# Kernel optimization log

Measured on AMD Instinct MI355X. Metric: run time of the kernel, lower is better.

Reference implementation:

```python
import jax, jax.numpy as jnp
import numpy as np

B, E, N, D = 1024, 64, 32, 64  # batch, entities, sampled neighbors, dim


def setup_inputs() -> dict:
    key = jax.random.key(0)
    ks = jax.random.split(key, 6)
    return {
        "self_vectors": jax.random.normal(ks[0], (B, E, 1, D), dtype=jnp.float32),
        "neighbor_vectors": jax.random.normal(ks[1], (B, E, N, D), dtype=jnp.float32),
        "neighbor_relations": jax.random.normal(ks[2], (B, E, N, D), dtype=jnp.float32),
        "user_embeddings": jax.random.normal(ks[3], (B, D), dtype=jnp.float32),
        "W": jax.random.normal(ks[4], (D, 2 * D), dtype=jnp.float32) * (1.0 / np.sqrt(2 * D)),
        "b": jax.random.normal(ks[5], (D,), dtype=jnp.float32) * 0.01,
    }


def reference(self_vectors, neighbor_vectors, neighbor_relations, user_embeddings, W, b):
    # per-neighbor relation scores: (u . r) over dim -> [B, E, N]
    scores = jnp.einsum("bd,bend->ben", user_embeddings, neighbor_relations)
    p = jax.nn.softmax(scores, axis=-1)  # over neighbors
    # weighted neighbor sum -> [B, E, D]
    neighbors_agg = jnp.einsum("ben,bend->bed", p, neighbor_vectors)
    # 'concat' aggregator: cat(self, agg) on feature axis -> [B*E, 2D]
    sv = self_vectors.reshape(B, E, D)
    output = jnp.concatenate([sv, neighbors_agg], axis=-1).reshape(-1, 2 * D)
    output = output @ W.T + b  # Linear(2D -> D)
    return jax.nn.relu(output).reshape(B, -1, D)  # act = ReLU (inner KGCN layers)
```

## Files before the change

kernel.cpp:

```cpp
#include <hip/hip_runtime.h>
#include <math.h>

#define NB  1024
#define NE  64
#define NN  32
#define ND  64

__global__ __launch_bounds__(256) void kgcn_agg_kernel(
    const float* __restrict__ self_v,
    const float* __restrict__ nbr_v,
    const float* __restrict__ nbr_r,
    const float* __restrict__ user,
    const float* __restrict__ W,
    const float* __restrict__ bias,
    float* __restrict__ out)
{
    const int pair = blockIdx.x;
    const int b    = pair >> 6;
    const int t    = threadIdx.x;

    __shared__ float4 s_u4[16];
    __shared__ float4 s_x4[32];
    __shared__ float  s_scores[NN];
    __shared__ float  s_p[NN];
    __shared__ float4 s_part4[256];

    float* s_u    = (float*)s_u4;
    float* s_x    = (float*)s_x4;
    float* s_part = (float*)s_part4;

    if (t < 64) {
        s_u[t] = user[b * ND + t];
    } else if (t < 128) {
        s_x[t - 64] = self_v[(size_t)pair * ND + (t - 64)];
    }
    __syncthreads();

    const float4* rel4 = (const float4*)(nbr_r + (size_t)pair * (NN * ND));
    const float4* nv4  = (const float4*)(nbr_v + (size_t)pair * (NN * ND));

    const int col = t & 15;
    const int rg  = t >> 4;
    const int n_a = rg;
    const int n_b = rg + 16;

    float4 u4 = s_u4[col];

    float4 ra = rel4[t];
    float4 rb = rel4[t + 256];
    float4 va = nv4[t];
    float4 vb = nv4[t + 256];

    float pa = ra.x * u4.x + ra.y * u4.y + ra.z * u4.z + ra.w * u4.w;
    float pb = rb.x * u4.x + rb.y * u4.y + rb.z * u4.z + rb.w * u4.w;

    #pragma unroll
    for (int off = 8; off > 0; off >>= 1) {
        pa += __shfl_down(pa, off, 16);
        pb += __shfl_down(pb, off, 16);
    }
    if (col == 0) {
        s_scores[n_a] = pa;
        s_scores[n_b] = pb;
    }
    __syncthreads();

    if (t < 32) {
        float v = s_scores[t];
        float m = v;
        #pragma unroll
        for (int off = 16; off > 0; off >>= 1)
            m = fmaxf(m, __shfl_xor(m, off, 32));
        float e = __expf(v - m);
        float s = e;
        #pragma unroll
        for (int off = 16; off > 0; off >>= 1)
            s += __shfl_xor(s, off, 32);
        s_p[t] = e / s;
    }
    __syncthreads();

    float p_a = s_p[n_a];
    float p_b = s_p[n_b];
    float4 acc;
    acc.x = p_a * va.x + p_b * vb.x;
    acc.y = p_a * va.y + p_b * vb.y;
    acc.z = p_a * va.z + p_b * vb.z;
    acc.w = p_a * va.w + p_b * vb.w;
    s_part4[rg * 16 + col] = acc;
    __syncthreads();

    if (t < 64) {
        float a = 0.f;
        #pragma unroll
        for (int g = 0; g < 16; ++g)
            a += s_part[g * 64 + t];
        s_x[64 + t] = a;
    }
    __syncthreads();

    const int dout = t >> 2;
    const int q    = t & 3;
    const float4* W4 = (const float4*)W;
    float acc2 = 0.f;
    #pragma unroll
    for (int i = 0; i < 8; ++i) {
        float4 w = W4[dout * 32 + q * 8 + i];
        float4 x = s_x4[q * 8 + i];
        acc2 += w.x * x.x + w.y * x.y + w.z * x.z + w.w * x.w;
    }
    acc2 += __shfl_down(acc2, 2, 4);
    acc2 += __shfl_down(acc2, 1, 4);
    if (q == 0) {
        float r = acc2 + bias[dout];
        out[(size_t)pair * ND + dout] = fmaxf(r, 0.f);
    }
}

extern "C" void kernel_launch(void* const* d_in, const int* in_sizes, int n_in,
                              void* d_out, int out_size, void* d_ws, size_t ws_size,
                              hipStream_t stream) {
    const float* self_v = (const float*)d_in[0];
    const float* nbr_v  = (const float*)d_in[1];
    const float* nbr_r  = (const float*)d_in[2];
    const float* user   = (const float*)d_in[3];
    const float* W      = (const float*)d_in[4];
    const float* bias   = (const float*)d_in[5];
    float* out          = (float*)d_out;

    const int n_pairs = NB * NE;
    kgcn_agg_kernel<<<n_pairs, 256, 0, stream>>>(
        self_v, nbr_v, nbr_r, user, W, bias, out);
}
```

Before: 1.097 ms.

## Map one wavefront per entity pair and drop block-level barriers

Each 64-lane wavefront now handles one (batch, entity) pair, with four pairs per 256-thread block. Scores, softmax and the weighted sum are done in registers with cross-lane shuffles instead of shared-memory staging and several __syncthreads. Each lane loads 16 float4 values, which raises memory-level parallelism but also register pressure. The linear layer has each lane compute one output over the full 128-length row of W, so each lane reads a whole W row rather than a quarter of one.

```diff
diff --git a/kernel.cpp b/kernel.cpp
--- a/kernel.cpp
+++ b/kernel.cpp
@@ -1,12 +1,13 @@
 #include <hip/hip_runtime.h>
 #include <math.h>
 
-#define NB  1024
-#define NE  64
-#define NN  32
-#define ND  64
+#define NB 1024
+#define NE 64
+#define NN 32
+#define ND 64
+#define PAIRS (NB * NE)
 
-__global__ __launch_bounds__(256) void kgcn_agg_kernel(
+__global__ __launch_bounds__(256) void kgcn_wave_kernel(
     const float* __restrict__ self_v,
     const float* __restrict__ nbr_v,
     const float* __restrict__ nbr_r,
@@ -15,106 +16,83 @@
     const float* __restrict__ bias,
     float* __restrict__ out)
 {
-    const int pair = blockIdx.x;
+    const int t    = threadIdx.x;
+    const int wv   = t >> 6;
+    const int ln   = t & 63;
+    const int pair = blockIdx.x * 4 + wv;
     const int b    = pair >> 6;
-    const int t    = threadIdx.x;
 
-    __shared__ float4 s_u4[16];
-    __shared__ float4 s_x4[32];
-    __shared__ float  s_scores[NN];
-    __shared__ float  s_p[NN];
-    __shared__ float4 s_part4[256];
+    const int g = ln >> 4;
+    const int c = ln & 15;
 
-    float* s_u    = (float*)s_u4;
-    float* s_x    = (float*)s_x4;
-    float* s_part = (float*)s_part4;
+    __shared__ float4 s_x4[4][32];
 
-    if (t < 64) {
-        s_u[t] = user[b * ND + t];
-    } else if (t < 128) {
-        s_x[t - 64] = self_v[(size_t)pair * ND + (t - 64)];
-    }
-    __syncthreads();
+    const float4* rel4  = (const float4*)(nbr_r + (size_t)pair * (NN * ND));
+    const float4* nv4   = (const float4*)(nbr_v + (size_t)pair * (NN * ND));
+    const float4* self4 = (const float4*)(self_v + (size_t)pair * ND);
+    const float4* user4 = (const float4*)(user + (size_t)b * ND);
 
-    const float4* rel4 = (const float4*)(nbr_r + (size_t)pair * (NN * ND));
-    const float4* nv4  = (const float4*)(nbr_v + (size_t)pair * (NN * ND));
+    if (ln < 16) s_x4[wv][ln] = self4[ln];
 
-    const int col = t & 15;
-    const int rg  = t >> 4;
-    const int n_a = rg;
-    const int n_b = rg + 16;
+    float4 u4 = user4[c];
 
-    float4 u4 = s_u4[col];
+    float4 ra[8], va[8];
+    #pragma unroll
+    for (int i = 0; i < 8; ++i) ra[i] = rel4[i * 64 + ln];
+    #pragma unroll
+    for (int i = 0; i < 8; ++i) va[i] = nv4[i * 64 + ln];
 
-    float4 ra = rel4[t];
-    float4 rb = rel4[t + 256];
-    float4 va = nv4[t];
-    float4 vb = nv4[t + 256];
-
-    float pa = ra.x * u4.x + ra.y * u4.y + ra.z * u4.z + ra.w * u4.w;
-    float pb = rb.x * u4.x + rb.y * u4.y + rb.z * u4.z + rb.w * u4.w;
+    float sc[8];
+    #pragma unroll
+    for (int i = 0; i < 8; ++i)
+        sc[i] = ra[i].x * u4.x + ra[i].y * u4.y + ra[i].z * u4.z + ra[i].w * u4.w;
 
     #pragma unroll
-    for (int off = 8; off > 0; off >>= 1) {
-        pa += __shfl_down(pa, off, 16);
-        pb += __shfl_down(pb, off, 16);
+    for (int off = 1; off < 16; off <<= 1) {
+        #pragma unroll
+        for (int i = 0; i < 8; ++i)
+            sc[i] += __shfl_xor(sc[i], off, 16);
     }
-    if (col == 0) {
-        s_scores[n_a] = pa;
-        s_scores[n_b] = pb;
-    }
-    __syncthreads();
 
-    if (t < 32) {
-        float v = s_scores[t];
-        float m = v;
-        #pragma unroll
-        for (int off = 16; off > 0; off >>= 1)
-            m = fmaxf(m, __shfl_xor(m, off, 32));
-        float e = __expf(v - m);
-        float s = e;
-        #pragma unroll
-        for (int off = 16; off > 0; off >>= 1)
-            s += __shfl_xor(s, off, 32);
-        s_p[t] = e / s;
-    }
-    __syncthreads();
+    float m = sc[0];
+    #pragma unroll
+    for (int i = 1; i < 8; ++i) m = fmaxf(m, sc[i]);
+    m = fmaxf(m, __shfl_xor(m, 16, 64));
+    m = fmaxf(m, __shfl_xor(m, 32, 64));
 
-    float p_a = s_p[n_a];
-    float p_b = s_p[n_b];
-    float4 acc;
-    acc.x = p_a * va.x + p_b * vb.x;
-    acc.y = p_a * va.y + p_b * vb.y;
-    acc.z = p_a * va.z + p_b * vb.z;
-    acc.w = p_a * va.w + p_b * vb.w;
-    s_part4[rg * 16 + col] = acc;
-    __syncthreads();
+    float e[8], s = 0.f;
+    #pragma unroll
+    for (int i = 0; i < 8; ++i) { e[i] = __expf(sc[i] - m); s += e[i]; }
+    s += __shfl_xor(s, 16, 64);
+    s += __shfl_xor(s, 32, 64);
+    const float inv = 1.f / s;
 
-    if (t < 64) {
-        float a = 0.f;
-        #pragma unroll
-        for (int g = 0; g < 16; ++g)
-            a += s_part[g * 64 + t];
-        s_x[64 + t] = a;
-    }
-    __syncthreads();
-
-    const int dout = t >> 2;
-    const int q    = t & 3;
-    const float4* W4 = (const float4*)W;
-    float acc2 = 0.f;
+    float4 acc = {0.f, 0.f, 0.f, 0.f};
     #pragma unroll
     for (int i = 0; i < 8; ++i) {
-        float4 w = W4[dout * 32 + q * 8 + i];
-        float4 x = s_x4[q * 8 + i];
-        acc2 += w.x * x.x + w.y * x.y + w.z * x.z + w.w * x.w;
+        const float p = e[i] * inv;
+        acc.x = fmaf(p, va[i].x, acc.x);
+        acc.y = fmaf(p, va[i].y, acc.y);
+        acc.z = fmaf(p, va[i].z, acc.z);
+        acc.w = fmaf(p, va[i].w, acc.w);
     }
-    acc2 += __shfl_down(acc2, 2, 4);
-    acc2 += __shfl_down(acc2, 1, 4);
-    if (q == 0) {
-        float r = acc2 + bias[dout];
-        out[(size_t)pair * ND + dout] = fmaxf(r, 0.f);
+    acc.x += __shfl_xor(acc.x, 16, 64); acc.x += __shfl_xor(acc.x, 32, 64);
+    acc.y += __shfl_xor(acc.y, 16, 64); acc.y += __shfl_xor(acc.y, 32, 64);
+    acc.z += __shfl_xor(acc.z, 16, 64); acc.z += __shfl_xor(acc.z, 32, 64);
+    acc.w += __shfl_xor(acc.w, 16, 64); acc.w += __shfl_xor(acc.w, 32, 64);
+
+    if (ln < 16) s_x4[wv][16 + ln] = acc;
+    __builtin_amdgcn_wave_barrier();
+
+    float accO = bias[ln];
+    const float4* Wr = (const float4*)W + ln * 32;
+    #pragma unroll
+    for (int k = 0; k < 32; ++k) {
+        float4 w = Wr[k];
+        float4 x = s_x4[wv][k];
+        accO = fmaf(w.x, x.x, fmaf(w.y, x.y, fmaf(w.z, x.z, fmaf(w.w, x.w, accO))));
     }
+    out[(size_t)pair * ND + ln] = fmaxf(accO, 0.f);
 }
 
 extern "C" void kernel_launch(void* const* d_in, const int* in_sizes, int n_in,
@@ -128,7 +106,6 @@
     const float* bias   = (const float*)d_in[5];
     float* out          = (float*)d_out;
 
-    const int n_pairs = NB * NE;
-    kgcn_agg_kernel<<<n_pairs, 256, 0, stream>>>(
+    kgcn_wave_kernel<<<PAIRS / 4, 256, 0, stream>>>(
         self_v, nbr_v, nbr_r, user, W, bias, out);
 }
```

New measurement: 1.126 ms. +2.7%, slower.
